# Kernel optimization log

Hardware: AMD Instinct MI355X
Metric: run time of the kernel (lower is better)

The kernel has to match this reference:

```python
import jax, jax.numpy as jnp
import numpy as np

NEG_INF = -1e30

def setup_inputs() -> dict:
    key = jax.random.key(0)
    k1, k2, k3, k4, k5 = jax.random.split(key, 5)
    B, N, Fin, Fout, H = 8, 1024, 128, 64, 4
    h = jax.random.normal(k1, (B, N, Fin), dtype=jnp.float32)
    adj = jax.random.randint(k2, (N, N), 0, 2, dtype=jnp.int32)
    bias_matrix = jax.random.normal(k3, (1, 1, N, N), dtype=jnp.float32)
    # xavier-ish scaled params
    W = jax.random.normal(k4, (H, Fin, Fout), dtype=jnp.float32) * (1.0 / np.sqrt(Fin))
    a = jax.random.normal(k5, (H, 2 * Fout, 1), dtype=jnp.float32) * (1.0 / np.sqrt(2 * Fout))
    return {"h": h, "adj": adj, "bias_matrix": bias_matrix, "W": W, "a": a}


def reference(h, adj, bias_matrix, W, a):
    B, N, _ = h.shape
    H, _, Fout = W.shape
    # h_prime: [B, N, H, Fout]
    h_prime = jnp.einsum('bni,hio->bnho', h, W)
    # split attention vector: a_input @ a == h_i @ a1 + h_j @ a2 (same math, no O(N^2*F) tensor)
    a1 = a[:, :Fout, 0]   # [H, Fout]
    a2 = a[:, Fout:, 0]   # [H, Fout]
    ei = jnp.einsum('bnhf,hf->bnh', h_prime, a1)  # [B, N, H]
    ej = jnp.einsum('bnhf,hf->bnh', h_prime, a2)  # [B, N, H]
    e = jax.nn.leaky_relu(ei[:, :, None, :] + ej[:, None, :, :], negative_slope=0.2)  # [B,N,N,H]
    # bias_matrix [1,1,N,N] -> expand to [B,1,N,N] -> permute(0,2,3,1) -> [B,N,N,1]
    bias = jnp.transpose(bias_matrix, (0, 2, 3, 1))  # [1, N, N, 1], broadcasts to [B,N,N,H]
    e = e + bias
    mask = (adj != 0)[None, :, :, None]  # [1, N, N, 1]
    e_masked = jnp.where(mask, e, NEG_INF)
    attention = jax.nn.softmax(e_masked, axis=2)  # softmax over j
    h_out = jnp.einsum('bijh,bjhf->bihf', attention, h_prime)  # [B, N, H, Fout]
    return h_out.reshape(B, N, H * Fout)
```

## Files before the change

### kernel.cpp

```cpp
#include <hip/hip_runtime.h>

constexpr int B = 8, N = 1024, FIN = 128, FOUT = 64, H = 4;
constexpr float LOG2E = 1.44269504f;

typedef __attribute__((ext_vector_type(8))) short short8;
typedef __attribute__((ext_vector_type(4))) short short4v;
typedef __attribute__((ext_vector_type(4))) float f32x4;

static __device__ inline unsigned short f2bf(float x) {
    union { float f; unsigned u; } v; v.f = x;
    unsigned r = v.u + 0x7fff + ((v.u >> 16) & 1);
    return (unsigned short)(r >> 16);
}

__global__ __launch_bounds__(256) void gat_prep(
    const float* __restrict__ h,
    const float* __restrict__ W,
    const float* __restrict__ a,
    const int*   __restrict__ adj,
    const float* __restrict__ bias,
    unsigned short* __restrict__ hpF,
    unsigned short* __restrict__ mbB,
    float* __restrict__ ei_t,
    float* __restrict__ ej_t)
{
    __shared__ float h_lds[16][132];
    const int t = threadIdx.x;

    if (blockIdx.x < 512) {
        const int bx   = blockIdx.x;
        const int ti   = bx >> 3;
        const int jc   = (bx & 7) * 4 + (t >> 6);
        const int lane = t & 63;
        const int i    = ti * 16 + (lane & 15);
        const int j0   = jc * 32 + 8 * (lane >> 4);

        const int4*   ap = reinterpret_cast<const int4*>(adj + (size_t)i * N + j0);
        const float4* bp = reinterpret_cast<const float4*>(bias + (size_t)i * N + j0);
        int4   a0 = ap[0], a1 = ap[1];
        float4 b0 = bp[0], b1 = bp[1];
        unsigned short q0 = f2bf(a0.x ? LOG2E * b0.x : -1e35f);
        unsigned short q1 = f2bf(a0.y ? LOG2E * b0.y : -1e35f);
        unsigned short q2 = f2bf(a0.z ? LOG2E * b0.z : -1e35f);
        unsigned short q3 = f2bf(a0.w ? LOG2E * b0.w : -1e35f);
        unsigned short q4 = f2bf(a1.x ? LOG2E * b1.x : -1e35f);
        unsigned short q5 = f2bf(a1.y ? LOG2E * b1.y : -1e35f);
        unsigned short q6 = f2bf(a1.z ? LOG2E * b1.z : -1e35f);
        unsigned short q7 = f2bf(a1.w ? LOG2E * b1.w : -1e35f);
        int4 ov;
        ov.x = (int)((unsigned)q0 | ((unsigned)q1 << 16));
        ov.y = (int)((unsigned)q2 | ((unsigned)q3 << 16));
        ov.z = (int)((unsigned)q4 | ((unsigned)q5 << 16));
        ov.w = (int)((unsigned)q6 | ((unsigned)q7 << 16));
        *reinterpret_cast<int4*>(mbB + (((size_t)ti * 32 + jc) * 64 + lane) * 8) = ov;
        return;
    }

    const int blk = blockIdx.x - 512;
    const int b   = blk >> 6;
    const int n0  = (blk & 63) * 16;

    {
        const float* src = h + ((size_t)b * N + n0) * FIN;
        for (int v = t; v < 512; v += 256) {
            float4 x = reinterpret_cast<const float4*>(src)[v];
            int fl = v * 4;
            *reinterpret_cast<float4*>(&h_lds[fl >> 7][fl & 127]) = x;
        }
    }
    __syncthreads();

    const int hd   = t >> 6;
    const int lane = t & 63;
    const int li   = lane & 15;
    const int f0   = li * 4;
    const int rg   = lane >> 4;

    float acc[4][4];
    #pragma unroll
    for (int k = 0; k < 4; ++k)
        #pragma unroll
        for (int j = 0; j < 4; ++j) acc[k][j] = 0.f;

    const float* Wp = W + (size_t)hd * FIN * FOUT + f0;
    #pragma unroll 8
    for (int i = 0; i < FIN; ++i) {
        float4 w4 = *reinterpret_cast<const float4*>(Wp + (size_t)i * FOUT);
        #pragma unroll
        for (int k = 0; k < 4; ++k) {
            float hv = h_lds[4 * rg + k][i];
            acc[k][0] = fmaf(hv, w4.x, acc[k][0]);
            acc[k][1] = fmaf(hv, w4.y, acc[k][1]);
            acc[k][2] = fmaf(hv, w4.z, acc[k][2]);
            acc[k][3] = fmaf(hv, w4.w, acc[k][3]);
        }
    }

    const int bh = b * H + hd;
    {
        const int na  = n0 + 4 * rg;
        const int jc  = na >> 5;
        const int kgn = (na >> 3) & 3;
        const int ft  = li >> 2;
        const int e0  = na & 4;
        #pragma unroll
        for (int jj = 0; jj < 4; ++jj) {
            short4v v4;
            v4[0] = (short)f2bf(acc[0][jj]);
            v4[1] = (short)f2bf(acc[1][jj]);
            v4[2] = (short)f2bf(acc[2][jj]);
            v4[3] = (short)f2bf(acc[3][jj]);
            const int lanep = (4 * (li & 3) + jj) + 16 * kgn;
            *reinterpret_cast<short4v*>(
                hpF + ((((size_t)bh * 32 + jc) * 4 + ft) * 64 + lanep) * 8 + e0) = v4;
        }
    }

    float4 a1 = *reinterpret_cast<const float4*>(a + (size_t)hd * 2 * FOUT + f0);
    float4 a2 = *reinterpret_cast<const float4*>(a + (size_t)hd * 2 * FOUT + FOUT + f0);
    #pragma unroll
    for (int k = 0; k < 4; ++k) {
        float e1 = acc[k][0] * a1.x + acc[k][1] * a1.y + acc[k][2] * a1.z + acc[k][3] * a1.w;
        float e2 = acc[k][0] * a2.x + acc[k][1] * a2.y + acc[k][2] * a2.z + acc[k][3] * a2.w;
        #pragma unroll
        for (int m = 1; m < 16; m <<= 1) {
            e1 += __shfl_xor(e1, m, 64);
            e2 += __shfl_xor(e2, m, 64);
        }
        if (li == 0) {
            int r = n0 + 4 * rg + k;
            ei_t[(size_t)bh * N + r] = LOG2E * e1;
            ej_t[(size_t)bh * N + r] = LOG2E * e2;
        }
    }
}

__global__ __launch_bounds__(512) void gat_attn(
    const unsigned short* __restrict__ hpF,
    const float* __restrict__ ei_t,
    const float* __restrict__ ej_t,
    const unsigned short* __restrict__ mbB,
    float* __restrict__ out)
{
    __shared__ __align__(16) char smem[24576];
    typedef unsigned short hstage_t[2][4][512];
    hstage_t* hstage = reinterpret_cast<hstage_t*>(smem);

    const int raw  = blockIdx.x;
    const int xcd  = raw & 7;
    const int k_   = raw >> 3;
    const int bh   = ((xcd >> 1) << 3) | (k_ >> 3);
    const int it0  = (((xcd & 1) << 3) | (k_ & 7)) * 4;
    const int t    = threadIdx.x;
    const int w8   = t >> 6;
    const int w    = w8 & 3;
    const int jh   = w8 >> 2;
    const int lane = t & 63;
    const int li   = lane & 15;
    const int kg   = lane >> 4;
    const int ti   = it0 + w;
    const int irow = ti * 16 + li;
    const int jcb  = jh * 16;

    const float  ei0   = ei_t[(size_t)bh * N + irow];
    const float* ejrow = ej_t + (size_t)bh * N;
    const unsigned short* mrow = mbB + ((size_t)ti * 32 * 64 + lane) * 8;
    const size_t hbase = (size_t)bh * 65536;

    f32x4 c0 = {0.f,0.f,0.f,0.f}, c1 = {0.f,0.f,0.f,0.f};
    f32x4 c2 = {0.f,0.f,0.f,0.f}, c3 = {0.f,0.f,0.f,0.f};
    f32x4 c4 = {0.f,0.f,0.f,0.f};
    const short obf = (short)0x3F80;
    const short8 ones = {obf,obf,obf,obf,obf,obf,obf,obf};

    #define VMCNT4() asm volatile("s_waitcnt vmcnt(4)" ::: "memory")
    #define BARRIER() { __builtin_amdgcn_s_barrier(); asm volatile("" ::: "memory"); }

    #define STAGE(BUF, JCG) {                                                 \
        const unsigned short* gs_ = hpF + hbase + (size_t)(JCG) * 2048        \
                                        + (size_t)w * 512 + (size_t)lane * 8; \
        __builtin_amdgcn_global_load_lds(                                     \
            (const __attribute__((address_space(1))) void*)gs_,               \
            (__attribute__((address_space(3))) void*)&hstage[BUF][jh][w][0],  \
            16, 0, 0); }

    #define REGS(S, JCG) {                                                    \
        mq##S  = *reinterpret_cast<const int4*>(mrow + (size_t)(JCG) * 512);  \
        ejA##S = *reinterpret_cast<const float4*>(ejrow + (JCG) * 32 + 8 * kg);\
        ejB##S = *reinterpret_cast<const float4*>(ejrow + (JCG) * 32 + 8 * kg + 4); }

    #define DSREAD(BUF, BA, BB, BC, BD) {                                     \
        BA = *reinterpret_cast<const short8*>(&hstage[BUF][jh][0][lane * 8]); \
        BB = *reinterpret_cast<const short8*>(&hstage[BUF][jh][1][lane * 8]); \
        BC = *reinterpret_cast<const short8*>(&hstage[BUF][jh][2][lane * 8]); \
        BD = *reinterpret_cast<const short8*>(&hstage[BUF][jh][3][lane * 8]); }

    #define SCORE2(PL, PH, EJL, EJH, QW) {                                    \
        float bl_ = __uint_as_float(((unsigned)(QW)) << 16);                  \
        float bh_ = __uint_as_float(((unsigned)(QW)) & 0xffff0000u);          \
        float el_ = ei0 + (EJL); el_ = fmaxf(el_, 0.2f * el_) + bl_;          \
        float eh_ = ei0 + (EJH); eh_ = fmaxf(eh_, 0.2f * eh_) + bh_;          \
        asm("v_exp_f32 %0, %1" : "=v"(PL) : "v"(el_));                        \
        asm("v_exp_f32 %0, %1" : "=v"(PH) : "v"(eh_)); }

    #define COMPS(S, BA, BB, BC, BD) {                                        \
        float p0,p1,p2,p3,p4,p5,p6,p7;                                        \
        SCORE2(p0, p1, ejA##S.x, ejA##S.y, mq##S.x)                           \
        SCORE2(p2, p3, ejA##S.z, ejA##S.w, mq##S.y)                           \
        SCORE2(p4, p5, ejB##S.x, ejB##S.y, mq##S.z)                           \
        SCORE2(p6, p7, ejB##S.z, ejB##S.w, mq##S.w)                           \
        int4 pk_;                                                             \
        asm("v_cvt_pk_bf16_f32 %0, %1, %2" : "=v"(pk_.x) : "v"(p0), "v"(p1)); \
        asm("v_cvt_pk_bf16_f32 %0, %1, %2" : "=v"(pk_.y) : "v"(p2), "v"(p3)); \
        asm("v_cvt_pk_bf16_f32 %0, %1, %2" : "=v"(pk_.z) : "v"(p4), "v"(p5)); \
        asm("v_cvt_pk_bf16_f32 %0, %1, %2" : "=v"(pk_.w) : "v"(p6), "v"(p7)); \
        short8 a0_ = *reinterpret_cast<short8*>(&pk_);                        \
        c0 = __builtin_amdgcn_mfma_f32_16x16x32_bf16(a0_, BA, c0, 0, 0, 0);   \
        c1 = __builtin_amdgcn_mfma_f32_16x16x32_bf16(a0_, BB, c1, 0, 0, 0);   \
        c2 = __builtin_amdgcn_mfma_f32_16x16x32_bf16(a0_, BC, c2, 0, 0, 0);   \
        c3 = __builtin_amdgcn_mfma_f32_16x16x32_bf16(a0_, BD, c3, 0, 0, 0);   \
        c4 = __builtin_amdgcn_mfma_f32_16x16x32_bf16(a0_, ones, c4, 0, 0, 0); }

    short8 A0, B0, C0, D0, A1, B1, C1, D1;
    int4 mq0, mq1;
    float4 ejA0, ejB0, ejA1, ejB1;

    STAGE(0, jcb + 0)
    STAGE(1, jcb + 1)
    REGS(0, jcb + 0)
    VMCNT4();
    BARRIER();

    int ba = 0, bb = 1;
    #pragma unroll 1
    for (int k = 0; k < 16; k += 2) {
        const int p2 = (k + 2 < 16) ? jcb + k + 2 : jcb + 15;
        const int p3 = (k + 3 < 16) ? jcb + k + 3 : jcb + 15;
        const int bn0 = ba == 0 ? 2 : (ba == 1 ? 0 : 1);
        const int bn1 = bb == 0 ? 2 : (bb == 1 ? 0 : 1);
        STAGE(bn0, p2)
        REGS(1, jcb + k + 1)
        DSREAD(ba, A0, B0, C0, D0)
        COMPS(0, A0, B0, C0, D0)
        VMCNT4();
        BARRIER();
        STAGE(bn1, p3)
        REGS(0, p2)
        DSREAD(bb, A1, B1, C1, D1)
        COMPS(1, A1, B1, C1, D1)
        VMCNT4();
        BARRIER();
        ba = bn0; bb = bn1;
    }
    #undef VMCNT4
    #undef BARRIER
    #undef STAGE
    #undef REGS
    #undef DSREAD
    #undef SCORE2
    #undef COMPS

    f32x4 (*red)[4][64] = reinterpret_cast<f32x4 (*)[4][64]>(smem);

    __syncthreads();
    if (jh == 1) {
        red[0][w][lane] = c0;
        red[1][w][lane] = c1;
        red[2][w][lane] = c2;
        red[3][w][lane] = c3;
        red[4][w][lane] = c4;
    }
    __syncthreads();
    if (jh == 1) return;

    c0 += red[0][w][lane];
    c1 += red[1][w][lane];
    c2 += red[2][w][lane];
    c3 += red[3][w][lane];
    c4 += red[4][w][lane];

    const int b  = bh >> 2;
    const int hd = bh & 3;
    #pragma unroll
    for (int r = 0; r < 4; ++r) {
        int orow = ti * 16 + 4 * kg + r;
        float inv = 1.0f / c4[r];
        float* ob = out + (((size_t)b * N + orow) * H + hd) * 64 + li;
        ob[0]  = c0[r] * inv;
        ob[16] = c1[r] * inv;
        ob[32] = c2[r] * inv;
        ob[48] = c3[r] * inv;
    }
}

extern "C" void kernel_launch(void* const* d_in, const int* in_sizes, int n_in,
                              void* d_out, int out_size, void* d_ws, size_t ws_size,
                              hipStream_t stream) {
    const float* h    = (const float*)d_in[0];
    const int*   adj  = (const int*)  d_in[1];
    const float* bias = (const float*)d_in[2];
    const float* W    = (const float*)d_in[3];
    const float* a    = (const float*)d_in[4];
    float* out = (float*)d_out;

    char* ws = (char*)d_ws;
    unsigned short* hpF = (unsigned short*)ws;
    unsigned short* mbB = (unsigned short*)(ws + ((size_t)4 << 20));
    float* ei_t = (float*)(ws + ((size_t)6 << 20));
    float* ej_t = ei_t + (size_t)B * H * N;

    gat_prep<<<512 + B * N / 16, 256, 0, stream>>>(h, W, a, adj, bias,
                                                   hpF, mbB, ei_t, ej_t);
    gat_attn<<<B * H * (N / 64), 512, 0, stream>>>(hpF, ei_t, ej_t, mbB, out);
}
```

Before: 35.80 us.

## Switch attention loop to four-buffer staging with one barrier per two chunks

```diff
diff --git a/kernel.cpp b/kernel.cpp
--- a/kernel.cpp
+++ b/kernel.cpp
@@ -142,7 +142,7 @@
     const unsigned short* __restrict__ mbB,
     float* __restrict__ out)
 {
-    __shared__ __align__(16) char smem[24576];
+    __shared__ __align__(16) char smem[32768];
     typedef unsigned short hstage_t[2][4][512];
     hstage_t* hstage = reinterpret_cast<hstage_t*>(smem);
 
@@ -173,7 +173,7 @@
     const short obf = (short)0x3F80;
     const short8 ones = {obf,obf,obf,obf,obf,obf,obf,obf};
 
-    #define VMCNT4() asm volatile("s_waitcnt vmcnt(4)" ::: "memory")
+    #define VMCNT6() asm volatile("s_waitcnt vmcnt(6)" ::: "memory")
     #define BARRIER() { __builtin_amdgcn_s_barrier(); asm volatile("" ::: "memory"); }
 
     #define STAGE(BUF, JCG) {                                                 \
@@ -228,31 +228,30 @@
     STAGE(0, jcb + 0)
     STAGE(1, jcb + 1)
     REGS(0, jcb + 0)
-    VMCNT4();
+    REGS(1, jcb + 1)
+    VMCNT6();
     BARRIER();
 
-    int ba = 0, bb = 1;
     #pragma unroll 1
     for (int k = 0; k < 16; k += 2) {
-        const int p2 = (k + 2 < 16) ? jcb + k + 2 : jcb + 15;
-        const int p3 = (k + 3 < 16) ? jcb + k + 3 : jcb + 15;
-        const int bn0 = ba == 0 ? 2 : (ba == 1 ? 0 : 1);
-        const int bn1 = bb == 0 ? 2 : (bb == 1 ? 0 : 1);
-        STAGE(bn0, p2)
-        REGS(1, jcb + k + 1)
+        const int pa = (k + 2 < 16) ? jcb + k + 2 : jcb + 15;
+        const int pb = (k + 3 < 16) ? jcb + k + 3 : jcb + 15;
+        const int ba = k & 2 ? 2 : 0;
+        const int bb = ba + 1;
+        const int bn0 = ba ^ 2;
+        const int bn1 = bb ^ 2;
+        STAGE(bn0, pa)
+        STAGE(bn1, pb)
         DSREAD(ba, A0, B0, C0, D0)
         COMPS(0, A0, B0, C0, D0)
-        VMCNT4();
-        BARRIER();
-        STAGE(bn1, p3)
-        REGS(0, p2)
+        REGS(0, pa)
         DSREAD(bb, A1, B1, C1, D1)
         COMPS(1, A1, B1, C1, D1)
-        VMCNT4();
+        REGS(1, pb)
+        VMCNT6();
         BARRIER();
-        ba = bn0; bb = bn1;
-    }
-    #undef VMCNT4
+    }
+    #undef VMCNT6
     #undef BARRIER
     #undef STAGE
     #undef REGS
```

After: 35.24 us. No clear change (-1.6%).
